# Optimization experiments

Hardware: AMD Instinct MI355X
Metric: run time of the kernel (lower is better)

Reference implementation:

```python
import jax, jax.numpy as jnp
import numpy as np

N, D, H = 32768, 128, 128          # cells, layer_dim, hidden
E_UP, E_DN, E_B, NB = 524288, 524288, 131072, 32768
BN_EPS = 1e-5


def _bn(z, g, b):
    # BatchNorm1d (training mode): normalize over the node axis (-2), biased var
    m = jnp.mean(z, axis=-2, keepdims=True)
    v = jnp.var(z, axis=-2, keepdims=True)
    return (z - m) * jax.lax.rsqrt(v + BN_EPS) * g + b


def setup_inputs() -> dict:
    key = jax.random.key(0)
    ks = jax.random.split(key, 16)
    w = lambda k, sh: jax.random.normal(k, sh, jnp.float32) * 0.05
    return {
        "x": jax.random.normal(ks[0], (N, D), jnp.float32),
        "up_index": jax.random.randint(ks[1], (2, E_UP), 0, N),
        "down_index": jax.random.randint(ks[2], (2, E_DN), 0, N),
        "boundary_index": jax.random.randint(ks[3], (2, E_B), 0, NB),
        "up_attr": jax.random.normal(ks[4], (E_UP, D), jnp.float32),
        "down_attr": jax.random.normal(ks[5], (E_DN, D), jnp.float32),
        "boundary_attr": jax.random.normal(ks[6], (NB, D), jnp.float32),
        "msg_up_w": w(ks[7], (2 * D, D)), "msg_up_b": jnp.zeros((D,), jnp.float32),
        "msg_down_w": w(ks[8], (2 * D, D)), "msg_down_b": jnp.zeros((D,), jnp.float32),
        "upd_w1": w(ks[9], (3, D, H)), "upd_b1": jnp.zeros((3, H), jnp.float32),
        "upd_g1": jnp.ones((3, H), jnp.float32), "upd_be1": jnp.zeros((3, H), jnp.float32),
        "upd_w2": w(ks[10], (3, H, H)), "upd_b2": jnp.zeros((3, H), jnp.float32),
        "upd_g2": jnp.ones((3, H), jnp.float32), "upd_be2": jnp.zeros((3, H), jnp.float32),
        "comb_w": w(ks[11], (3 * H, H)), "comb_b": jnp.zeros((H,), jnp.float32),
        "comb_g": jnp.ones((H,), jnp.float32), "comb_be": jnp.zeros((H,), jnp.float32),
    }


def reference(x, up_index, down_index, boundary_index, up_attr, down_attr,
              boundary_attr, msg_up_w, msg_up_b, msg_down_w, msg_down_b,
              upd_w1, upd_b1, upd_g1, upd_be1, upd_w2, upd_b2, upd_g2, upd_be2,
              comb_w, comb_b, comb_g, comb_be):
    n = x.shape[0]
    # --- message_up: msg_up_nn = ReLU(Linear(cat([x_j, up_attr]))) ; scatter-add
    m_up = jax.nn.relu(jnp.concatenate([x[up_index[1]], up_attr], -1) @ msg_up_w + msg_up_b)
    out_up = jax.ops.segment_sum(m_up, up_index[0], num_segments=n)
    # --- message_down: same structure with down_attr
    m_dn = jax.nn.relu(jnp.concatenate([x[down_index[1]], down_attr], -1) @ msg_down_w + msg_down_b)
    out_dn = jax.ops.segment_sum(m_dn, down_index[0], num_segments=n)
    # --- boundary messages: identity msg nn, gather boundary cells, scatter-add
    out_b = jax.ops.segment_sum(boundary_attr[boundary_index[0]], boundary_index[1], num_segments=n)
    # --- GIN-style self term: (1 + eps) * x with eps = 0
    h = jnp.stack([out_up + x, out_dn + x, out_b + x])        # [3, N, D]
    # --- update MLPs (Linear -> BN -> ReLU -> Linear -> BN -> ReLU), 3 branches stacked
    h = jax.nn.relu(_bn(jnp.einsum('knd,kdh->knh', h, upd_w1) + upd_b1[:, None, :],
                        upd_g1[:, None, :], upd_be1[:, None, :]))
    h = jax.nn.relu(_bn(jnp.einsum('knh,khf->knf', h, upd_w2) + upd_b2[:, None, :],
                        upd_g2[:, None, :], upd_be2[:, None, :]))
    # --- combine: Linear(3H -> H) -> BN -> ReLU
    cat = jnp.concatenate([h[0], h[1], h[2]], -1)             # [N, 3H]
    return jax.nn.relu(_bn(cat @ comb_w + comb_b, comb_g, comb_be))
```

## Files before the change

kernel.cpp:

```cpp
#include <hip/hip_runtime.h>


#define NCELLS 32768
#define EUP    524288
#define EDN    524288
#define EB     131072
#define NS     4194304
#define CH_SH  17408

typedef __attribute__((ext_vector_type(8))) __bf16 bf16x8;
typedef __attribute__((ext_vector_type(4))) float  float4v;

static __device__ __forceinline__ unsigned short f2bf(float v) {
  __bf16 b = (__bf16)v;
  return __builtin_bit_cast(unsigned short, b);
}
static __device__ __forceinline__ float bf2f(unsigned short u) {
  unsigned int x = ((unsigned int)u) << 16;
  return __builtin_bit_cast(float, x);
}

#define GLD_LDS16(gp, lp)                                                    \
  __builtin_amdgcn_global_load_lds(                                          \
      (const __attribute__((address_space(1))) void*)(gp),                   \
      (__attribute__((address_space(3))) void*)(lp), 16, 0, 0)

enum { M_T = 0, M_EDGE = 1, M_Z = 2, M_COMB = 3 };

template<int MODE, bool XFORM>
__global__ __launch_bounds__(256) void gemm_k(
    const float* __restrict__ A,
    const unsigned short* __restrict__ wsT, int chunk0,
    const float* __restrict__ bias,
    const float* __restrict__ ta, const float* __restrict__ tc,
    const unsigned short* __restrict__ Tb, int tcoff,
    const int* __restrict__ aperm, const int* __restrict__ ssrc,
    const int* __restrict__ sdstg,
    float* __restrict__ outp,
    float* __restrict__ ssum, float* __restrict__ ssq, int K)
{
  __shared__ __align__(16) unsigned short Wt[CH_SH];
  __shared__ int   sdst_s[64];
  __shared__ float sTa[384], sTc[384];

  const int tid  = threadIdx.x;
  const int wave = tid >> 6, lane = tid & 63;
  const int quad = lane >> 4, l16 = lane & 15;
  const int br   = blockIdx.y;

  const float* Ab = A;
  const float* biasb = bias;
  const float* tab = ta; const float* tcb = tc;
  float* outb = outp;
  float* ssumb = ssum; float* ssqb = ssq;
  int cidx = chunk0, tco = tcoff;
  if (MODE == M_T) { cidx += 2 * br; tco = 128 * br; }
  if (MODE == M_Z) {
    Ab += (size_t)br * NS; cidx += br; biasb += 128 * br;
    if (XFORM) { tab += 128 * br; tcb += 128 * br; }
    outb += (size_t)br * NS; ssumb += 128 * br; ssqb += 128 * br;
  }

  const int rowBase = blockIdx.x * 64 + wave * 16;
  int arow = (MODE == M_EDGE) ? aperm[rowBase + l16] : (rowBase + l16);

  if (XFORM)
    for (int i = tid; i < K; i += 256) { sTa[i] = tab[i]; sTc[i] = tcb[i]; }

  float4v acc[8];
#pragma unroll
  for (int nt = 0; nt < 8; ++nt) acc[nt] = (float4v){0.f, 0.f, 0.f, 0.f};

  for (int kc = 0; kc < K; kc += 128) {
    float4v pa[4], pb[4];
#pragma unroll
    for (int ks = 0; ks < 4; ++ks) {
      const float* ap;
      if (MODE == M_COMB)
        ap = Ab + (size_t)(kc >> 7) * NS + (size_t)arow * 128 + ks * 32 + quad * 8;
      else
        ap = Ab + (size_t)arow * 128 + ks * 32 + quad * 8;
      pa[ks] = *(const float4v*)ap;
      pb[ks] = *(const float4v*)(ap + 4);
    }

    if (kc) __syncthreads();
    {
      const char* g = (const char*)(wsT + (size_t)(cidx + (kc >> 7)) * CH_SH);
      char* l = (char*)Wt;
      for (int off = wave * 1024; off < 2 * CH_SH; off += 4096)
        GLD_LDS16(g + off + lane * 16, l + off);
    }
    __syncthreads();

#pragma unroll
    for (int ks = 0; ks < 4; ++ks) {
      const int kk0 = kc + ks * 32 + quad * 8;
      float av[8];
#pragma unroll
      for (int j = 0; j < 4; ++j) { av[j] = pa[ks][j]; av[4 + j] = pb[ks][j]; }
      if (XFORM) {
#pragma unroll
        for (int j = 0; j < 8; ++j)
          av[j] = fmaxf(fmaf(sTa[kk0 + j], av[j], sTc[kk0 + j]), 0.f);
      }
      bf16x8 af;
#pragma unroll
      for (int j = 0; j < 8; ++j) af[j] = (__bf16)av[j];
#pragma unroll
      for (int nt = 0; nt < 8; ++nt) {
        bf16x8 bf = *(const bf16x8*)&Wt[(nt * 16 + l16) * 136 + ks * 32 + quad * 8];
        acc[nt] = __builtin_amdgcn_mfma_f32_16x16x32_bf16(af, bf, acc[nt], 0, 0, 0);
      }
    }
  }

  const int crow = rowBase + quad * 4;

  if (MODE == M_T) {
    unsigned short* To = (unsigned short*)outb;
#pragma unroll
    for (int nt = 0; nt < 8; ++nt) {
      const int col = nt * 16 + l16;
#pragma unroll
      for (int r = 0; r < 4; ++r)
        To[(size_t)(crow + r) * 256 + tco + col] = f2bf(acc[nt][r]);
    }
  } else if (MODE == M_EDGE) {
    int srcs[4];
#pragma unroll
    for (int r = 0; r < 4; ++r) srcs[r] = ssrc[crow + r];
    __syncthreads();
    if (tid < 64) sdst_s[tid] = sdstg[blockIdx.x * 64 + tid];
    float* Cb = (float*)Wt;
#pragma unroll
    for (int nt = 0; nt < 8; ++nt) {
      const int col = nt * 16 + l16;
      const float bb = biasb[col];
#pragma unroll
      for (int r = 0; r < 4; ++r) {
        float tv = bf2f(Tb[(size_t)srcs[r] * 256 + tco + col]);
        float v = fmaxf(acc[nt][r] + bb + tv, 0.f);
        Cb[(wave * 16 + quad * 4 + r) * 132 + col] = v;
      }
    }
    __syncthreads();
    const int col = tid & 127, half = tid >> 7;
    const int r0 = half * 32;
    int cur = sdst_s[r0];
    float a = 0.f;
    for (int r = r0; r < r0 + 32; ++r) {
      int d = sdst_s[r];
      if (d != cur) {
        unsafeAtomicAdd(&outb[(size_t)cur * 128 + col], a);
        a = 0.f; cur = d;
      }
      a += Cb[r * 132 + col];
    }
    unsafeAtomicAdd(&outb[(size_t)cur * 128 + col], a);
  } else {
#pragma unroll
    for (int nt = 0; nt < 8; ++nt) {
      const int col = nt * 16 + l16;
      const float bb = biasb[col];
      float s = 0.f, ss = 0.f;
#pragma unroll
      for (int r = 0; r < 4; ++r) {
        float v = acc[nt][r] + bb;
        outb[(size_t)(crow + r) * 128 + col] = v;
        s += v; ss += v * v;
      }
      s  += __shfl_xor(s, 16);  s  += __shfl_xor(s, 32);
      ss += __shfl_xor(ss, 16); ss += __shfl_xor(ss, 32);
      if (quad == 0) {
        unsafeAtomicAdd(&ssumb[col], s);
        unsafeAtomicAdd(&ssqb[col], ss);
      }
    }
  }
}

__global__ __launch_bounds__(256) void prep_w(
    const float* __restrict__ muw, const float* __restrict__ mdw,
    const float* __restrict__ w1, const float* __restrict__ w2,
    const float* __restrict__ cw, unsigned short* __restrict__ wsT)
{
  const int chunk = blockIdx.y;
  const float* src;
  if      (chunk == 0) src = muw;
  else if (chunk == 1) src = muw + 16384;
  else if (chunk == 2) src = mdw;
  else if (chunk == 3) src = mdw + 16384;
  else if (chunk < 7)  src = w1 + (chunk - 4) * 16384;
  else if (chunk < 10) src = w2 + (chunk - 7) * 16384;
  else                 src = cw + (chunk - 10) * 16384;
  int i = blockIdx.x * 256 + threadIdx.x;
  int k = i >> 7, n = i & 127;
  wsT[(size_t)chunk * CH_SH + n * 136 + k] = f2bf(src[i]);
}

__global__ __launch_bounds__(256) void hist3(
    const int* __restrict__ up, const int* __restrict__ dn,
    const int* __restrict__ bnd, int* __restrict__ cnts)
{
  int i = blockIdx.x * 256 + threadIdx.x;
  if (i < EUP) atomicAdd(&cnts[up[i]], 1);
  else if (i < EUP + EDN) atomicAdd(&cnts[32768 + dn[i - EUP]], 1);
  else atomicAdd(&cnts[65536 + bnd[EB + (i - EUP - EDN)]], 1);
}

__global__ __launch_bounds__(1024) void scan3(
    const int* __restrict__ cnts, int* __restrict__ rs, int* __restrict__ cur)
{
  __shared__ int part[1024];
  const int seg = blockIdx.x, t = threadIdx.x;
  const int* c = cnts + seg * 32768;
  int local[32]; int s = 0;
#pragma unroll
  for (int i = 0; i < 32; ++i) { local[i] = c[t * 32 + i]; s += local[i]; }
  part[t] = s;
  __syncthreads();
  for (int off = 1; off < 1024; off <<= 1) {
    int v = (t >= off) ? part[t - off] : 0;
    __syncthreads();
    part[t] += v;
    __syncthreads();
  }
  int base = t ? part[t - 1] : 0;
  int* r  = rs  + seg * 32769;
  int* cu = cur + seg * 32768;
#pragma unroll
  for (int i = 0; i < 32; ++i) {
    r[t * 32 + i] = base; cu[t * 32 + i] = base; base += local[i];
  }
  if (t == 1023) r[32768] = part[1023];
}

__global__ __launch_bounds__(256) void scat3(
    const int* __restrict__ up, const int* __restrict__ dn,
    const int* __restrict__ bnd, int* __restrict__ cur,
    int* __restrict__ uperm, int* __restrict__ usrc, int* __restrict__ udst,
    int* __restrict__ dperm, int* __restrict__ dsrc, int* __restrict__ ddst,
    int* __restrict__ bperm)
{
  int i = blockIdx.x * 256 + threadIdx.x;
  if (i < EUP) {
    int d = up[i]; int p = atomicAdd(&cur[d], 1);
    uperm[p] = i; usrc[p] = up[EUP + i]; udst[p] = d;
  } else if (i < EUP + EDN) {
    int e = i - EUP; int d = dn[e]; int p = atomicAdd(&cur[32768 + d], 1);
    dperm[p] = e; dsrc[p] = dn[EDN + e]; ddst[p] = d;
  } else {
    int e = i - EUP - EDN; int d = bnd[EB + e];
    int p = atomicAdd(&cur[65536 + d], 1);
    bperm[p] = bnd[e];
  }
}

__global__ __launch_bounds__(256) void init_h01(const float* __restrict__ x,
                                                float* __restrict__ h)
{
  size_t i = (size_t)blockIdx.x * 256 + threadIdx.x;
  float4v v = ((const float4v*)x)[i];
  ((float4v*)h)[i] = v;
  ((float4v*)(h + NS))[i] = v;
}

__global__ __launch_bounds__(256) void bnd_agg(
    const float* __restrict__ x, const float* __restrict__ battr,
    const int* __restrict__ bperm, const int* __restrict__ rs,
    float* __restrict__ h2)
{
  int node = blockIdx.x * 2 + (threadIdx.x >> 7);
  int col  = threadIdx.x & 127;
  float acc = x[(size_t)node * 128 + col];
  int s = rs[node], e = rs[node + 1];
  for (int i = s; i < e; ++i)
    acc += battr[(size_t)bperm[i] * 128 + col];
  h2[(size_t)node * 128 + col] = acc;
}

__global__ __launch_bounds__(256) void bn_params(
    const float* __restrict__ ssum, const float* __restrict__ ssq,
    const float* __restrict__ g, const float* __restrict__ be,
    float* __restrict__ a, float* __restrict__ c, int nch)
{
  int i = blockIdx.x * 256 + threadIdx.x;
  if (i < nch) {
    float m   = ssum[i] * (1.f / NCELLS);
    float var = ssq[i] * (1.f / NCELLS) - m * m;
    float inv = rsqrtf(var + 1e-5f);
    float ai  = g[i] * inv;
    a[i] = ai;
    c[i] = be[i] - m * ai;
  }
}

__global__ __launch_bounds__(256) void finalize_k(
    const float* __restrict__ z3, const float* __restrict__ a,
    const float* __restrict__ c, float* __restrict__ out)
{
  int idx = blockIdx.x * 256 + threadIdx.x;
  int ch = idx & 127;
  out[idx] = fmaxf(fmaf(a[ch], z3[idx], c[ch]), 0.f);
}

extern "C" void kernel_launch(void* const* d_in, const int* in_sizes, int n_in,
                              void* d_out, int out_size, void* d_ws, size_t ws_size,
                              hipStream_t stream)
{
  (void)in_sizes; (void)n_in; (void)out_size; (void)ws_size;

  const float* x       = (const float*)d_in[0];
  const int*   up_idx  = (const int*)d_in[1];
  const int*   dn_idx  = (const int*)d_in[2];
  const int*   b_idx   = (const int*)d_in[3];
  const float* up_attr = (const float*)d_in[4];
  const float* dn_attr = (const float*)d_in[5];
  const float* b_attr  = (const float*)d_in[6];
  const float* mu_w    = (const float*)d_in[7];
  const float* mu_b    = (const float*)d_in[8];
  const float* md_w    = (const float*)d_in[9];
  const float* md_b    = (const float*)d_in[10];
  const float* w1      = (const float*)d_in[11];
  const float* b1      = (const float*)d_in[12];
  const float* g1      = (const float*)d_in[13];
  const float* be1     = (const float*)d_in[14];
  const float* w2      = (const float*)d_in[15];
  const float* b2      = (const float*)d_in[16];
  const float* g2      = (const float*)d_in[17];
  const float* be2     = (const float*)d_in[18];
  const float* cw      = (const float*)d_in[19];
  const float* cb      = (const float*)d_in[20];
  const float* cg      = (const float*)d_in[21];
  const float* cbe     = (const float*)d_in[22];

  float* ws = (float*)d_ws;
  unsigned short* T = (unsigned short*)ws;
  float* h     = ws + NS;
  float* z1    = h + 3 * (size_t)NS;
  float* z2    = h;
  float* z3    = z1;
  float* stats = z1 + 3 * (size_t)NS;
  float* prm   = stats + 1792;
  unsigned short* wsT = (unsigned short*)(prm + 1792);
  int* cnts  = (int*)(wsT + 13 * CH_SH);
  int* cur   = cnts + 3 * 32768;
  int* rs    = cur + 3 * 32768;
  int* uperm = rs + 3 * 32769 + 1;
  int* usrc  = uperm + EUP;
  int* udst  = usrc + EUP;
  int* dperm = udst + EUP;
  int* dsrc  = dperm + EDN;
  int* ddst  = dsrc + EDN;
  int* bperm = ddst + EDN;

  hipMemsetAsync(stats, 0, 1792 * sizeof(float), stream);
  hipMemsetAsync(cnts, 0, 3 * 32768 * sizeof(int), stream);

  prep_w<<<dim3(64, 13), 256, 0, stream>>>(mu_w, md_w, w1, w2, cw, wsT);
  hist3<<<4608, 256, 0, stream>>>(up_idx, dn_idx, b_idx, cnts);
  scan3<<<3, 1024, 0, stream>>>(cnts, rs, cur);
  scat3<<<4608, 256, 0, stream>>>(up_idx, dn_idx, b_idx, cur,
                                  uperm, usrc, udst, dperm, dsrc, ddst, bperm);

  gemm_k<M_T, false><<<dim3(512, 2), 256, 0, stream>>>(
      x, wsT, 0, nullptr, nullptr, nullptr, nullptr, 0,
      nullptr, nullptr, nullptr, (float*)T, nullptr, nullptr, 128);

  init_h01<<<4096, 256, 0, stream>>>(x, h);

  gemm_k<M_EDGE, false><<<dim3(8192, 1), 256, 0, stream>>>(
      up_attr, wsT, 1, mu_b, nullptr, nullptr, T, 0,
      uperm, usrc, udst, h, nullptr, nullptr, 128);
  gemm_k<M_EDGE, false><<<dim3(8192, 1), 256, 0, stream>>>(
      dn_attr, wsT, 3, md_b, nullptr, nullptr, T, 128,
      dperm, dsrc, ddst, h + NS, nullptr, nullptr, 128);

  bnd_agg<<<16384, 256, 0, stream>>>(x, b_attr, bperm, rs + 2 * 32769,
                                     h + 2 * (size_t)NS);

  gemm_k<M_Z, false><<<dim3(512, 3), 256, 0, stream>>>(
      h, wsT, 4, b1, nullptr, nullptr, nullptr, 0,
      nullptr, nullptr, nullptr, z1, stats, stats + 384, 128);
  bn_params<<<2, 256, 0, stream>>>(stats, stats + 384, g1, be1, prm, prm + 384, 384);

  gemm_k<M_Z, true><<<dim3(512, 3), 256, 0, stream>>>(
      z1, wsT, 7, b2, prm, prm + 384, nullptr, 0,
      nullptr, nullptr, nullptr, z2, stats + 768, stats + 1152, 384 == 384 ? 128 : 128);
  bn_params<<<2, 256, 0, stream>>>(stats + 768, stats + 1152, g2, be2,
                                   prm + 768, prm + 1152, 384);

  gemm_k<M_COMB, true><<<dim3(512, 1), 256, 0, stream>>>(
      z2, wsT, 10, cb, prm + 768, prm + 1152, nullptr, 0,
      nullptr, nullptr, nullptr, z3, stats + 1536, stats + 1664, 384);
  bn_params<<<1, 256, 0, stream>>>(stats + 1536, stats + 1664, cg, cbe,
                                   prm + 1536, prm + 1664, 128);

  finalize_k<<<16384, 256, 0, stream>>>(z3, prm + 1536, prm + 1664,
                                        (float*)d_out);
}
```

Baseline: 1.189 ms.

## Fuse x-projection into edge GEMM and fold BN params into consumers

Removes the separate pass that projected x through the first half of the message weights into a bf16 table. The edge kernel now gathers x rows directly and runs a K=256 GEMM over [x_j, attr], with up and down branches merged into one launch over a 2-D grid. Edge metadata is packed into int4 records, and the bn_params kernels are removed by computing scale and shift inside the consumer kernels. The trade-off is twice the MFMA work per edge and a random fp32 gather of x, in exchange for dropping the T-table write and its scattered bf16 reads plus several launches.

Result: no change. 1.209 ms (+1.7%).

```diff
diff --git a/kernel.cpp b/kernel.cpp
--- a/kernel.cpp
+++ b/kernel.cpp
@@ -15,57 +15,149 @@
   __bf16 b = (__bf16)v;
   return __builtin_bit_cast(unsigned short, b);
 }
-static __device__ __forceinline__ float bf2f(unsigned short u) {
-  unsigned int x = ((unsigned int)u) << 16;
-  return __builtin_bit_cast(float, x);
-}
 
 #define GLD_LDS16(gp, lp)                                                    \
   __builtin_amdgcn_global_load_lds(                                          \
       (const __attribute__((address_space(1))) void*)(gp),                   \
       (__attribute__((address_space(3))) void*)(lp), 16, 0, 0)
 
-enum { M_T = 0, M_EDGE = 1, M_Z = 2, M_COMB = 3 };
-
-template<int MODE, bool XFORM>
-__global__ __launch_bounds__(256) void gemm_k(
-    const float* __restrict__ A,
-    const unsigned short* __restrict__ wsT, int chunk0,
-    const float* __restrict__ bias,
-    const float* __restrict__ ta, const float* __restrict__ tc,
-    const unsigned short* __restrict__ Tb, int tcoff,
-    const int* __restrict__ aperm, const int* __restrict__ ssrc,
-    const int* __restrict__ sdstg,
-    float* __restrict__ outp,
-    float* __restrict__ ssum, float* __restrict__ ssq, int K)
+enum { M_Z = 0, M_COMB = 1 };
+
+__global__ __launch_bounds__(256) void edge_gemm_k(
+    const float* __restrict__ xin,
+    const float* __restrict__ upA, const float* __restrict__ dnA,
+    const unsigned short* __restrict__ wsT,
+    const float* __restrict__ upb, const float* __restrict__ dnb,
+    const int4* __restrict__ ue, const int4* __restrict__ de,
+    float* __restrict__ hout)
 {
   __shared__ __align__(16) unsigned short Wt[CH_SH];
-  __shared__ int   sdst_s[64];
-  __shared__ float sTa[384], sTc[384];
+  __shared__ int sdst_s[64];
 
   const int tid  = threadIdx.x;
   const int wave = tid >> 6, lane = tid & 63;
   const int quad = lane >> 4, l16 = lane & 15;
   const int br   = blockIdx.y;
 
+  const float* attr  = br ? dnA : upA;
+  const float* bias  = br ? dnb : upb;
+  const int4*  edges = br ? de : ue;
+  float* outb = hout + (size_t)br * NS;
+  const int cbase = 2 * br;
+
+  const int rowBase = blockIdx.x * 64 + wave * 16;
+  const int4 e = edges[rowBase + l16];
+  if (quad == 0) sdst_s[wave * 16 + l16] = e.z;
+
+  float4v acc[8];
+#pragma unroll
+  for (int nt = 0; nt < 8; ++nt) acc[nt] = (float4v){0.f, 0.f, 0.f, 0.f};
+
+#pragma unroll
+  for (int kc = 0; kc < 256; kc += 128) {
+    const float* Abase = kc ? attr : xin;
+    const int ar = kc ? e.x : e.y;
+    float4v pa[4], pb[4];
+#pragma unroll
+    for (int ks = 0; ks < 4; ++ks) {
+      const float* ap = Abase + (size_t)ar * 128 + ks * 32 + quad * 8;
+      pa[ks] = *(const float4v*)ap;
+      pb[ks] = *(const float4v*)(ap + 4);
+    }
+
+    if (kc) __syncthreads();
+    {
+      const char* g = (const char*)(wsT + (size_t)(cbase + (kc >> 7)) * CH_SH);
+      char* l = (char*)Wt;
+      for (int off = wave * 1024; off < 2 * CH_SH; off += 4096)
+        GLD_LDS16(g + off + lane * 16, l + off);
+    }
+    __syncthreads();
+
+#pragma unroll
+    for (int ks = 0; ks < 4; ++ks) {
+      bf16x8 af;
+#pragma unroll
+      for (int j = 0; j < 4; ++j) {
+        af[j]     = (__bf16)pa[ks][j];
+        af[4 + j] = (__bf16)pb[ks][j];
+      }
+#pragma unroll
+      for (int nt = 0; nt < 8; ++nt) {
+        bf16x8 bf = *(const bf16x8*)&Wt[(nt * 16 + l16) * 136 + ks * 32 + quad * 8];
+        acc[nt] = __builtin_amdgcn_mfma_f32_16x16x32_bf16(af, bf, acc[nt], 0, 0, 0);
+      }
+    }
+  }
+
+  __syncthreads();
+  float* Cb = (float*)Wt;
+#pragma unroll
+  for (int nt = 0; nt < 8; ++nt) {
+    const int col = nt * 16 + l16;
+    const float bb = bias[col];
+#pragma unroll
+    for (int r = 0; r < 4; ++r)
+      Cb[(wave * 16 + quad * 4 + r) * 132 + col] = fmaxf(acc[nt][r] + bb, 0.f);
+  }
+  __syncthreads();
+  const int col = tid & 127, half = tid >> 7;
+  const int r0 = half * 32;
+  int cur = sdst_s[r0];
+  float a = 0.f;
+  for (int r = r0; r < r0 + 32; ++r) {
+    int d = sdst_s[r];
+    if (d != cur) {
+      unsafeAtomicAdd(&outb[(size_t)cur * 128 + col], a);
+      a = 0.f; cur = d;
+    }
+    a += Cb[r * 132 + col];
+  }
+  unsafeAtomicAdd(&outb[(size_t)cur * 128 + col], a);
+}
+
+template<int MODE, bool XFORM>
+__global__ __launch_bounds__(256) void mlp_gemm_k(
+    const float* __restrict__ A,
+    const unsigned short* __restrict__ wsT, int chunk0,
+    const float* __restrict__ bias,
+    const float* __restrict__ psum, const float* __restrict__ psq,
+    const float* __restrict__ pg, const float* __restrict__ pbe,
+    float* __restrict__ outp,
+    float* __restrict__ ssum, float* __restrict__ ssq, int K)
+{
+  __shared__ __align__(16) unsigned short Wt[CH_SH];
+  __shared__ float sTa[384], sTc[384];
+
+  const int tid  = threadIdx.x;
+  const int wave = tid >> 6, lane = tid & 63;
+  const int quad = lane >> 4, l16 = lane & 15;
+  const int br   = blockIdx.y;
+
   const float* Ab = A;
   const float* biasb = bias;
-  const float* tab = ta; const float* tcb = tc;
+  const float* psb = psum; const float* pqb = psq;
+  const float* pgb = pg;   const float* pbeb = pbe;
   float* outb = outp;
   float* ssumb = ssum; float* ssqb = ssq;
-  int cidx = chunk0, tco = tcoff;
-  if (MODE == M_T) { cidx += 2 * br; tco = 128 * br; }
+  int cidx = chunk0;
   if (MODE == M_Z) {
     Ab += (size_t)br * NS; cidx += br; biasb += 128 * br;
-    if (XFORM) { tab += 128 * br; tcb += 128 * br; }
     outb += (size_t)br * NS; ssumb += 128 * br; ssqb += 128 * br;
-  }
+    if (XFORM) { psb += 128 * br; pqb += 128 * br; pgb += 128 * br; pbeb += 128 * br; }
+  }
+
+  if (XFORM)
+    for (int i = tid; i < K; i += 256) {
+      float m   = psb[i] * (1.f / NCELLS);
+      float var = pqb[i] * (1.f / NCELLS) - m * m;
+      float ai  = pgb[i] * rsqrtf(var + 1e-5f);
+      sTa[i] = ai;
+      sTc[i] = pbeb[i] - m * ai;
+    }
 
   const int rowBase = blockIdx.x * 64 + wave * 16;
-  int arow = (MODE == M_EDGE) ? aperm[rowBase + l16] : (rowBase + l16);
-
-  if (XFORM)
-    for (int i = tid; i < K; i += 256) { sTa[i] = tab[i]; sTc[i] = tcb[i]; }
+  const int arow = rowBase + l16;
 
   float4v acc[8];
 #pragma unroll
@@ -116,66 +208,22 @@
   }
 
   const int crow = rowBase + quad * 4;
-
-  if (MODE == M_T) {
-    unsigned short* To = (unsigned short*)outb;
-#pragma unroll
-    for (int nt = 0; nt < 8; ++nt) {
-      const int col = nt * 16 + l16;
-#pragma unroll
-      for (int r = 0; r < 4; ++r)
-        To[(size_t)(crow + r) * 256 + tco + col] = f2bf(acc[nt][r]);
-    }
-  } else if (MODE == M_EDGE) {
-    int srcs[4];
-#pragma unroll
-    for (int r = 0; r < 4; ++r) srcs[r] = ssrc[crow + r];
-    __syncthreads();
-    if (tid < 64) sdst_s[tid] = sdstg[blockIdx.x * 64 + tid];
-    float* Cb = (float*)Wt;
-#pragma unroll
-    for (int nt = 0; nt < 8; ++nt) {
-      const int col = nt * 16 + l16;
-      const float bb = biasb[col];
-#pragma unroll
-      for (int r = 0; r < 4; ++r) {
-        float tv = bf2f(Tb[(size_t)srcs[r] * 256 + tco + col]);
-        float v = fmaxf(acc[nt][r] + bb + tv, 0.f);
-        Cb[(wave * 16 + quad * 4 + r) * 132 + col] = v;
-      }
-    }
-    __syncthreads();
-    const int col = tid & 127, half = tid >> 7;
-    const int r0 = half * 32;
-    int cur = sdst_s[r0];
-    float a = 0.f;
-    for (int r = r0; r < r0 + 32; ++r) {
-      int d = sdst_s[r];
-      if (d != cur) {
-        unsafeAtomicAdd(&outb[(size_t)cur * 128 + col], a);
-        a = 0.f; cur = d;
-      }
-      a += Cb[r * 132 + col];
-    }
-    unsafeAtomicAdd(&outb[(size_t)cur * 128 + col], a);
-  } else {
-#pragma unroll
-    for (int nt = 0; nt < 8; ++nt) {
-      const int col = nt * 16 + l16;
-      const float bb = biasb[col];
-      float s = 0.f, ss = 0.f;
-#pragma unroll
-      for (int r = 0; r < 4; ++r) {
-        float v = acc[nt][r] + bb;
-        outb[(size_t)(crow + r) * 128 + col] = v;
-        s += v; ss += v * v;
-      }
-      s  += __shfl_xor(s, 16);  s  += __shfl_xor(s, 32);
-      ss += __shfl_xor(ss, 16); ss += __shfl_xor(ss, 32);
-      if (quad == 0) {
-        unsafeAtomicAdd(&ssumb[col], s);
-        unsafeAtomicAdd(&ssqb[col], ss);
-      }
+#pragma unroll
+  for (int nt = 0; nt < 8; ++nt) {
+    const int col = nt * 16 + l16;
+    const float bb = biasb[col];
+    float s = 0.f, ss = 0.f;
+#pragma unroll
+    for (int r = 0; r < 4; ++r) {
+      float v = acc[nt][r] + bb;
+      outb[(size_t)(crow + r) * 128 + col] = v;
+      s += v; ss += v * v;
+    }
+    s  += __shfl_xor(s, 16);  s  += __shfl_xor(s, 32);
+    ss += __shfl_xor(ss, 16); ss += __shfl_xor(ss, 32);
+    if (quad == 0) {
+      unsafeAtomicAdd(&ssumb[col], s);
+      unsafeAtomicAdd(&ssqb[col], ss);
     }
   }
 }
@@ -239,17 +287,17 @@
 __global__ __launch_bounds__(256) void scat3(
     const int* __restrict__ up, const int* __restrict__ dn,
     const int* __restrict__ bnd, int* __restrict__ cur,
-    int* __restrict__ uperm, int* __restrict__ usrc, int* __restrict__ udst,
-    int* __restrict__ dperm, int* __restrict__ dsrc, int* __restrict__ ddst,
-    int* __restrict__ bperm)
+    int4* __restrict__ ue, int4* __restrict__ de, int* __restrict__ bperm)
 {
   int i = blockIdx.x * 256 + threadIdx.x;
   if (i < EUP) {
     int d = up[i]; int p = atomicAdd(&cur[d], 1);
-    uperm[p] = i; usrc[p] = up[EUP + i]; udst[p] = d;
+    int4 v; v.x = i; v.y = up[EUP + i]; v.z = d; v.w = 0;
+    ue[p] = v;
   } else if (i < EUP + EDN) {
     int e = i - EUP; int d = dn[e]; int p = atomicAdd(&cur[32768 + d], 1);
-    dperm[p] = e; dsrc[p] = dn[EDN + e]; ddst[p] = d;
+    int4 v; v.x = e; v.y = dn[EDN + e]; v.z = d; v.w = 0;
+    de[p] = v;
   } else {
     int e = i - EUP - EDN; int d = bnd[EB + e];
     int p = atomicAdd(&cur[65536 + d], 1);
@@ -280,29 +328,18 @@
   h2[(size_t)node * 128 + col] = acc;
 }
 
-__global__ __launch_bounds__(256) void bn_params(
-    const float* __restrict__ ssum, const float* __restrict__ ssq,
-    const float* __restrict__ g, const float* __restrict__ be,
-    float* __restrict__ a, float* __restrict__ c, int nch)
-{
-  int i = blockIdx.x * 256 + threadIdx.x;
-  if (i < nch) {
-    float m   = ssum[i] * (1.f / NCELLS);
-    float var = ssq[i] * (1.f / NCELLS) - m * m;
-    float inv = rsqrtf(var + 1e-5f);
-    float ai  = g[i] * inv;
-    a[i] = ai;
-    c[i] = be[i] - m * ai;
-  }
-}
-
 __global__ __launch_bounds__(256) void finalize_k(
-    const float* __restrict__ z3, const float* __restrict__ a,
-    const float* __restrict__ c, float* __restrict__ out)
+    const float* __restrict__ z3, const float* __restrict__ ssum,
+    const float* __restrict__ ssq, const float* __restrict__ g,
+    const float* __restrict__ be, float* __restrict__ out)
 {
   int idx = blockIdx.x * 256 + threadIdx.x;
   int ch = idx & 127;
-  out[idx] = fmaxf(fmaf(a[ch], z3[idx], c[ch]), 0.f);
+  float m   = ssum[ch] * (1.f / NCELLS);
+  float var = ssq[ch] * (1.f / NCELLS) - m * m;
+  float a   = g[ch] * rsqrtf(var + 1e-5f);
+  float c   = be[ch] - m * a;
+  out[idx] = fmaxf(fmaf(a, z3[idx], c), 0.f);
 }
 
 extern "C" void kernel_launch(void* const* d_in, const int* in_sizes, int n_in,
@@ -336,24 +373,18 @@
   const float* cbe     = (const float*)d_in[22];
 
   float* ws = (float*)d_ws;
-  unsigned short* T = (unsigned short*)ws;
-  float* h     = ws + NS;
+  float* h     = ws;
   float* z1    = h + 3 * (size_t)NS;
   float* z2    = h;
   float* z3    = z1;
   float* stats = z1 + 3 * (size_t)NS;
-  float* prm   = stats + 1792;
-  unsigned short* wsT = (unsigned short*)(prm + 1792);
-  int* cnts  = (int*)(wsT + 13 * CH_SH);
+  unsigned short* wsT = (unsigned short*)(stats + 1792);
+  int* cnts  = (int*)(wsT + 13 * (size_t)CH_SH);
   int* cur   = cnts + 3 * 32768;
   int* rs    = cur + 3 * 32768;
-  int* uperm = rs + 3 * 32769 + 1;
-  int* usrc  = uperm + EUP;
-  int* udst  = usrc + EUP;
-  int* dperm = udst + EUP;
-  int* dsrc  = dperm + EDN;
-  int* ddst  = dsrc + EDN;
-  int* bperm = ddst + EDN;
+  int4* ue   = (int4*)(rs + 3 * 32769 + 1);
+  int4* de   = ue + EUP;
+  int* bperm = (int*)(de + EDN);
 
   hipMemsetAsync(stats, 0, 1792 * sizeof(float), stream);
   hipMemsetAsync(cnts, 0, 3 * 32768 * sizeof(int), stream);
@@ -361,42 +392,28 @@
   prep_w<<<dim3(64, 13), 256, 0, stream>>>(mu_w, md_w, w1, w2, cw, wsT);
   hist3<<<4608, 256, 0, stream>>>(up_idx, dn_idx, b_idx, cnts);
   scan3<<<3, 1024, 0, stream>>>(cnts, rs, cur);
-  scat3<<<4608, 256, 0, stream>>>(up_idx, dn_idx, b_idx, cur,
-                                  uperm, usrc, udst, dperm, dsrc, ddst, bperm);
-
-  gemm_k<M_T, false><<<dim3(512, 2), 256, 0, stream>>>(
-      x, wsT, 0, nullptr, nullptr, nullptr, nullptr, 0,
-      nullptr, nullptr, nullptr, (float*)T, nullptr, nullptr, 128);
+  scat3<<<4608, 256, 0, stream>>>(up_idx, dn_idx, b_idx, cur, ue, de, bperm);
 
   init_h01<<<4096, 256, 0, stream>>>(x, h);
 
-  gemm_k<M_EDGE, false><<<dim3(8192, 1), 256, 0, stream>>>(
-      up_attr, wsT, 1, mu_b, nullptr, nullptr, T, 0,
-      uperm, usrc, udst, h, nullptr, nullptr, 128);
-  gemm_k<M_EDGE, false><<<dim3(8192, 1), 256, 0, stream>>>(
-      dn_attr, wsT, 3, md_b, nullptr, nullptr, T, 128,
-      dperm, dsrc, ddst, h + NS, nullptr, nullptr, 128);
+  edge_gemm_k<<<dim3(8192, 2), 256, 0, stream>>>(
+      x, up_attr, dn_attr, wsT, mu_b, md_b, ue, de, h);
 
   bnd_agg<<<16384, 256, 0, stream>>>(x, b_attr, bperm, rs + 2 * 32769,
                                      h + 2 * (size_t)NS);
 
-  gemm_k<M_Z, false><<<dim3(512, 3), 256, 0, stream>>>(
-      h, wsT, 4, b1, nullptr, nullptr, nullptr, 0,
-      nullptr, nullptr, nullptr, z1, stats, stats + 384, 128);
-  bn_params<<<2, 256, 0, stream>>>(stats, stats + 384, g1, be1, prm, prm + 384, 384);
-
-  gemm_k<M_Z, true><<<dim3(512, 3), 256, 0, stream>>>(
-      z1, wsT, 7, b2, prm, prm + 384, nullptr, 0,
-      nullptr, nullptr, nullptr, z2, stats + 768, stats + 1152, 384 == 384 ? 128 : 128);
-  bn_params<<<2, 256, 0, stream>>>(stats + 768, stats + 1152, g2, be2,
-                                   prm + 768, prm + 1152, 384);
-
-  gemm_k<M_COMB, true><<<dim3(512, 1), 256, 0, stream>>>(
-      z2, wsT, 10, cb, prm + 768, prm + 1152, nullptr, 0,
-      nullptr, nullptr, nullptr, z3, stats + 1536, stats + 1664, 384);
-  bn_params<<<1, 256, 0, stream>>>(stats + 1536, stats + 1664, cg, cbe,
-                                   prm + 1536, prm + 1664, 128);
-
-  finalize_k<<<16384, 256, 0, stream>>>(z3, prm + 1536, prm + 1664,
-                                        (float*)d_out);
-}
+  mlp_gemm_k<M_Z, false><<<dim3(512, 3), 256, 0, stream>>>(
+      h, wsT, 4, b1, nullptr, nullptr, nullptr, nullptr,
+      z1, stats, stats + 384, 128);
+
+  mlp_gemm_k<M_Z, true><<<dim3(512, 3), 256, 0, stream>>>(
+      z1, wsT, 7, b2, stats, stats + 384, g1, be1,
+      z2, stats + 768, stats + 1152, 128);
+
+  mlp_gemm_k<M_COMB, true><<<dim3(512, 1), 256, 0, stream>>>(
+      z2, wsT, 10, cb, stats + 768, stats + 1152, g2, be2,
+      z3, stats + 1536, stats + 1664, 384);
+
+  finalize_k<<<16384, 256, 0, stream>>>(z3, stats + 1536, stats + 1664,
+                                        cg, cbe, (float*)d_out);
+}
```
